# Kernel optimization log

Measured on AMD Instinct MI355X. Metric: run time of the kernel, lower is better.

## Reference

```python
import jax, jax.numpy as jnp
import numpy as np

N_HEAD = 12
N_EMBD = 768

def setup_inputs() -> dict:
    key = jax.random.key(0)
    ks = jax.random.split(key, 5)
    B, T, C = 4, 2048, N_EMBD
    x = jax.random.normal(ks[0], (B, T, C), dtype=jnp.float32)
    # PyTorch Linear default init ~ U(-1/sqrt(fan_in), 1/sqrt(fan_in)); use small normals for a clean baseline
    s = 1.0 / np.sqrt(C)
    W_attn = jax.random.uniform(ks[1], (C, 3 * C), minval=-s, maxval=s, dtype=jnp.float32)
    b_attn = jax.random.uniform(ks[2], (3 * C,), minval=-s, maxval=s, dtype=jnp.float32)
    W_o = jax.random.uniform(ks[3], (C, C), minval=-s, maxval=s, dtype=jnp.float32)
    b_o = jax.random.uniform(ks[4], (C,), minval=-s, maxval=s, dtype=jnp.float32)
    return {"x": x, "W_attn": W_attn, "b_attn": b_attn, "W_o": W_o, "b_o": b_o}

def reference(x, W_attn, b_attn, W_o, b_o):
    B, T, C = x.shape
    H = N_HEAD
    D = C // H  # head dim
    qkv = x @ W_attn + b_attn                      # [B,T,3C]
    q, k, v = jnp.split(qkv, 3, axis=-1)           # each [B,T,C]
    q = q.reshape(B, T, H, D).transpose(0, 2, 1, 3)  # [B,H,T,D]
    k = k.reshape(B, T, H, D).transpose(0, 2, 1, 3)
    v = v.reshape(B, T, H, D).transpose(0, 2, 1, 3)
    att = jnp.einsum('bhqd,bhkd->bhqk', q, k) / jnp.sqrt(jnp.asarray(D, x.dtype))
    causal = jnp.tril(jnp.ones((T, T), dtype=bool))
    att = jnp.where(causal, att, jnp.asarray(-jnp.inf, att.dtype))
    att = jax.nn.softmax(att, axis=-1)             # dropout=0.0 -> identity
    y = jnp.einsum('bhqk,bhkd->bhqd', att, v)      # [B,H,T,D]
    y = y.transpose(0, 2, 1, 3).reshape(B, T, C)   # [B,T,C]
    return y @ W_o + b_o
```

## Files before the change

kernel.cpp:

```cpp
#include <hip/hip_runtime.h>
#include <hip/hip_bf16.h>

#define NHEAD 12
#define TSEQ 2048
#define CEMB 768
#define DHEAD 64
#define NBATCH 4

typedef __attribute__((ext_vector_type(8))) short bf16x8;
typedef __attribute__((ext_vector_type(4))) float f32x4;

__device__ __forceinline__ ushort f2bf(float f) {
  union { float f; unsigned u; } v; v.f = f;
  unsigned u = v.u;
  u += 0x7FFFu + ((u >> 16) & 1u);
  return (ushort)(u >> 16);
}

__device__ __forceinline__ unsigned cvt_pk_bf16(float lo, float hi) {
  unsigned r;
  asm("v_cvt_pk_bf16_f32 %0, %1, %2" : "=v"(r) : "v"(lo), "v"(hi));
  return r;
}

__device__ __forceinline__ float exp2_raw(float x) {
  float r;
  asm("v_exp_f32 %0, %1" : "=v"(r) : "v"(x));
  return r;
}

__global__ __launch_bounds__(256)
void prep(const float* __restrict__ x, ushort* __restrict__ xb,
          const float* __restrict__ Wa, ushort* __restrict__ WaT,
          const float* __restrict__ Wo, ushort* __restrict__ WoT)
{
  __shared__ float tile[32][33];
  const int bid = blockIdx.x, t = threadIdx.x;
  if (bid < 3072) {
    int i = (bid * 256 + t) * 8;
    float4 v0 = *(const float4*)(x + i);
    float4 v1 = *(const float4*)(x + i + 4);
    bf16x8 wv;
    wv[0] = (short)f2bf(v0.x); wv[1] = (short)f2bf(v0.y);
    wv[2] = (short)f2bf(v0.z); wv[3] = (short)f2bf(v0.w);
    wv[4] = (short)f2bf(v1.x); wv[5] = (short)f2bf(v1.y);
    wv[6] = (short)f2bf(v1.z); wv[7] = (short)f2bf(v1.w);
    *(bf16x8*)(xb + i) = wv;
    return;
  }
  const int b2 = bid - 3072;
  const int bx = b2 % 96, by = b2 / 96;
  const int tx = t & 31, ty = t >> 5;
  const float* src; ushort* dst; int C, c0;
  if (bx < 72) { src = Wa; dst = WaT; C = 3 * CEMB; c0 = bx * 32; }
  else         { src = Wo; dst = WoT; C = CEMB;     c0 = (bx - 72) * 32; }
  const int r0 = by * 32;
#pragma unroll
  for (int j = 0; j < 4; ++j)
    tile[ty + j * 8][tx] = src[(size_t)(r0 + ty + j * 8) * C + c0 + tx];
  __syncthreads();
#pragma unroll
  for (int j = 0; j < 4; ++j)
    dst[(size_t)(c0 + ty + j * 8) * CEMB + r0 + tx] = f2bf(tile[tx][ty + j * 8]);
}

template<int EPI>
__global__ __launch_bounds__(256)
void gemm_bf16(const ushort* __restrict__ A, const ushort* __restrict__ BT,
               const float* __restrict__ bias, float* __restrict__ outF,
               ushort* __restrict__ qd, ushort* __restrict__ kd, ushort* __restrict__ vd,
               int M, int N, int K)
{
  __shared__ __align__(16) char smem[32768];
  const int t = threadIdx.x;
  const int lane = t & 63, wv = t >> 6;
  const int cc = lane & 15, gg = lane >> 4;
  const int m0 = blockIdx.y * 128, n0 = blockIdx.x * 128;
  const int wm = (wv >> 1) * 64, wn = (wv & 1) * 64;

  const int o0 = wv * 1024 + lane * 16;
  const int o1 = o0 + 4096;
  const int r0s = o0 >> 6, s0s = (o0 >> 4) & 3;
  const int r1s = o1 >> 6, s1s = (o1 >> 4) & 3;
  const size_t Kb = (size_t)K * 2;
  const char* a0p = (const char*)A  + (size_t)(m0 + r0s) * Kb + ((s0s ^ ((r0s >> 1) & 3)) << 4);
  const char* a1p = (const char*)A  + (size_t)(m0 + r1s) * Kb + ((s1s ^ ((r1s >> 1) & 3)) << 4);
  const char* b0p = (const char*)BT + (size_t)(n0 + r0s) * Kb + ((s0s ^ ((r0s >> 1) & 3)) << 4);
  const char* b1p = (const char*)BT + (size_t)(n0 + r1s) * Kb + ((s1s ^ ((r1s >> 1) & 3)) << 4);

  auto stage_g = [&](int p, int kb) {
    char* As = smem + p * 16384;
    char* Bs = As + 8192;
    __builtin_amdgcn_global_load_lds(
        (const __attribute__((address_space(1))) unsigned*)(a0p + kb),
        (__attribute__((address_space(3))) unsigned*)(As + wv * 1024), 16, 0, 0);
    __builtin_amdgcn_global_load_lds(
        (const __attribute__((address_space(1))) unsigned*)(a1p + kb),
        (__attribute__((address_space(3))) unsigned*)(As + wv * 1024 + 4096), 16, 0, 0);
    __builtin_amdgcn_global_load_lds(
        (const __attribute__((address_space(1))) unsigned*)(b0p + kb),
        (__attribute__((address_space(3))) unsigned*)(Bs + wv * 1024), 16, 0, 0);
    __builtin_amdgcn_global_load_lds(
        (const __attribute__((address_space(1))) unsigned*)(b1p + kb),
        (__attribute__((address_space(3))) unsigned*)(Bs + wv * 1024 + 4096), 16, 0, 0);
  };

  f32x4 acc[4][4];
#pragma unroll
  for (int i = 0; i < 4; ++i)
#pragma unroll
    for (int j = 0; j < 4; ++j) acc[i][j] = (f32x4){0.f, 0.f, 0.f, 0.f};

  const int KB = K * 2;
  stage_g(0, 0);
  asm volatile("s_waitcnt vmcnt(0)" ::: "memory");
  __syncthreads();
  int p = 0;
  for (int kb = 0; kb < KB; kb += 64) {
    if (kb + 64 < KB) stage_g(p ^ 1, kb + 64);
    const char* As = smem + p * 16384;
    const char* Bs = As + 8192;
    bf16x8 fa[4], fb[4];
#pragma unroll
    for (int i = 0; i < 4; ++i) {
      const int r = wm + i * 16 + cc;
      fa[i] = *(const bf16x8*)(As + r * 64 + ((gg ^ ((r >> 1) & 3)) << 4));
    }
#pragma unroll
    for (int j = 0; j < 4; ++j) {
      const int r = wn + j * 16 + cc;
      fb[j] = *(const bf16x8*)(Bs + r * 64 + ((gg ^ ((r >> 1) & 3)) << 4));
    }
    __builtin_amdgcn_s_setprio(1);
#pragma unroll
    for (int i = 0; i < 4; ++i)
#pragma unroll
      for (int j = 0; j < 4; ++j)
        acc[i][j] = __builtin_amdgcn_mfma_f32_16x16x32_bf16(fa[i], fb[j], acc[i][j], 0, 0, 0);
    __builtin_amdgcn_s_setprio(0);
    asm volatile("s_waitcnt vmcnt(0)" ::: "memory");
    __syncthreads();
    p ^= 1;
  }

#pragma unroll
  for (int i = 0; i < 4; ++i) {
#pragma unroll
    for (int j = 0; j < 4; ++j) {
      int gm0 = m0 + wm + i * 16 + gg * 4;
      int gn  = n0 + wn + j * 16 + cc;
      float bv = bias[gn];
      if (EPI == 0) {
#pragma unroll
        for (int e = 0; e < 4; ++e)
          outF[(size_t)(gm0 + e) * N + gn] = acc[i][j][e] + bv;
      } else {
        int which = gn / CEMB;
        int r = gn - which * CEMB;
        int hh = r >> 6, dd = r & 63;
        int tt0 = gm0 & (TSEQ - 1), bb = gm0 >> 11;
        if (which == 2) {
          ushort* dstv = vd + ((size_t)((bb * NHEAD + hh) * DHEAD + dd)) * TSEQ + tt0;
          uint2 pw;
          pw.x = cvt_pk_bf16(acc[i][j][0] + bv, acc[i][j][1] + bv);
          pw.y = cvt_pk_bf16(acc[i][j][2] + bv, acc[i][j][3] + bv);
          *(uint2*)dstv = pw;
        } else {
          ushort* dst = which == 0 ? qd : kd;
          float sc = (which == 0) ? 0.125f * 1.4426950408889634f : 1.0f;
#pragma unroll
          for (int e = 0; e < 4; ++e)
            dst[(size_t)((bb * NHEAD + hh) * TSEQ + tt0 + e) * DHEAD + dd] =
                f2bf((acc[i][j][e] + bv) * sc);
        }
      }
    }
  }
}

__global__ __launch_bounds__(256)
void attn_fwd(const ushort* __restrict__ qg, const ushort* __restrict__ kg,
              const ushort* __restrict__ vTg, ushort* __restrict__ ybb)
{
  __shared__ __align__(16) char smem[49152];
  const int t = threadIdx.x, lane = t & 63, w = t >> 6;
  const int cc = lane & 15, gg = lane >> 4;
  const int NT = TSEQ / 64;
  const int L = blockIdx.x;
  const int r9 = L >> 3;
  const int bx = r9 & 15;
  const int bh = (L & 7) + 8 * (r9 >> 4);
  const int b = bh / NHEAD, h = bh - b * NHEAD;

  const char* Kg = (const char*)(kg + (size_t)bh * TSEQ * DHEAD);
  const char* Vg = (const char*)(vTg + (size_t)bh * TSEQ * DHEAD);

  const int srow = lane >> 3;
  const int ssw  = ((lane & 7) * 16) ^ (srow << 4);

  ushort* Pw = (ushort*)(smem + 32768 + w * 4096);
  const int sw8 = (cc & 7) << 3;

  auto stageK = [&](int pb, int kt) {
#pragma unroll
    for (int i = 0; i < 2; ++i) {
      const int c = w * 2 + i;
      const char* gk = Kg + (size_t)(kt * 64 + c * 8 + srow) * 128 + ssw;
      __builtin_amdgcn_global_load_lds(
          (const __attribute__((address_space(1))) unsigned*)gk,
          (__attribute__((address_space(3))) unsigned*)(smem + pb * 8192 + c * 1024),
          16, 0, 0);
    }
  };
  auto stageV = [&](int pb, int kt) {
#pragma unroll
    for (int i = 0; i < 2; ++i) {
      const int c = w * 2 + i;
      const char* gv = Vg + (size_t)(c * 8 + srow) * (TSEQ * 2) + (size_t)kt * 128 + ssw;
      __builtin_amdgcn_global_load_lds(
          (const __attribute__((address_space(1))) unsigned*)gv,
          (__attribute__((address_space(3))) unsigned*)(smem + 16384 + pb * 8192 + c * 1024),
          16, 0, 0);
    }
  };

  int p = 0;
  for (int pass = 0; pass < 2; ++pass) {
    const int qt = pass ? (NT - 1 - bx) : bx;
    const int qrow0 = qt * 64 + w * 16;

    const ushort* Qp = qg + ((size_t)bh * TSEQ + qrow0) * DHEAD;
    bf16x8 fq0 = *(const bf16x8*)(Qp + cc * DHEAD + 8 * gg);
    bf16x8 fq1 = *(const bf16x8*)(Qp + cc * DHEAD + 32 + 8 * gg);

    f32x4 o[4];
#pragma unroll
    for (int i = 0; i < 4; ++i) o[i] = (f32x4){0.f, 0.f, 0.f, 0.f};
    float m = -1e30f, l = 0.f;

    stageK(p, 0);
    asm volatile("s_waitcnt vmcnt(0)" ::: "memory");
    __syncthreads();

    for (int kt = 0; kt <= qt; ++kt) {
      if (kt < qt) stageK(p ^ 1, kt + 1);
      stageV(p, kt);

      const char* Kl = smem + p * 8192;
      f32x4 st[4];
#pragma unroll
      for (int ct = 0; ct < 4; ++ct) st[ct] = (f32x4){0.f, 0.f, 0.f, 0.f};
      __builtin_amdgcn_s_setprio(1);
#pragma unroll
      for (int ct = 0; ct < 4; ++ct) {
        const int r = ct * 16 + cc;
        const char* kb = Kl + r * 128;
        bf16x8 fk0 = *(const bf16x8*)(kb + ((gg * 16) ^ ((r & 7) << 4)));
        bf16x8 fk1 = *(const bf16x8*)(kb + ((64 + gg * 16) ^ ((r & 7) << 4)));
        st[ct] = __builtin_amdgcn_mfma_f32_16x16x32_bf16(fk0, fq0, st[ct], 0, 0, 0);
        st[ct] = __builtin_amdgcn_mfma_f32_16x16x32_bf16(fk1, fq1, st[ct], 0, 0, 0);
      }

      if (kt > 0) {
        const char* Vprev = smem + 16384 + (p ^ 1) * 8192;
        const ushort* Pprev = Pw + (p ^ 1) * 1024;
#pragma unroll
        for (int kc = 0; kc < 2; ++kc) {
          bf16x8 pb = *(const bf16x8*)&Pprev[cc * 64 + ((kc * 32 + 8 * gg) ^ sw8)];
#pragma unroll
          for (int dt = 0; dt < 4; ++dt) {
            const int rd = dt * 16 + cc;
            bf16x8 fv = *(const bf16x8*)(Vprev + rd * 128 + ((kc * 64 + gg * 16) ^ ((rd & 7) << 4)));
            o[dt] = __builtin_amdgcn_mfma_f32_16x16x32_bf16(fv, pb, o[dt], 0, 0, 0);
          }
        }
      }
      __builtin_amdgcn_s_setprio(0);

      if (kt == qt) {
#pragma unroll
        for (int ct = 0; ct < 4; ++ct)
#pragma unroll
          for (int e = 0; e < 4; ++e)
            if (ct * 16 + gg * 4 + e > w * 16 + cc) st[ct][e] = -1e30f;
      }
      float ml = st[0][0];
#pragma unroll
      for (int ct = 0; ct < 4; ++ct)
#pragma unroll
        for (int e = 0; e < 4; ++e) ml = fmaxf(ml, st[ct][e]);
      ml = fmaxf(ml, __shfl_xor(ml, 16, 64));
      ml = fmaxf(ml, __shfl_xor(ml, 32, 64));
      float mn = m;
      if (!__all(ml - m <= 11.54f)) {
        mn = fmaxf(m, ml);
        float al = exp2_raw(m - mn);
#pragma unroll
        for (int dt = 0; dt < 4; ++dt)
#pragma unroll
          for (int e = 0; e < 4; ++e) o[dt][e] *= al;
        l *= al;
        m = mn;
      }
      float ps = 0.f;
#pragma unroll
      for (int ct = 0; ct < 4; ++ct)
#pragma unroll
        for (int e = 0; e < 4; ++e) { float pp = exp2_raw(st[ct][e] - mn); st[ct][e] = pp; ps += pp; }
#pragma unroll
      for (int ct = 0; ct < 4; ++ct) {
        uint2 pw;
        pw.x = cvt_pk_bf16(st[ct][0], st[ct][1]);
        pw.y = cvt_pk_bf16(st[ct][2], st[ct][3]);
        *(uint2*)&Pw[p * 1024 + cc * 64 + ((ct * 16 + gg * 4) ^ sw8)] = pw;
      }
      ps += __shfl_xor(ps, 16, 64);
      ps += __shfl_xor(ps, 32, 64);
      l += ps;

      asm volatile("s_waitcnt vmcnt(0)" ::: "memory");
      __syncthreads();
      p ^= 1;
    }

    {
      const char* Vlast = smem + 16384 + (p ^ 1) * 8192;
      const ushort* Plast = Pw + (p ^ 1) * 1024;
#pragma unroll
      for (int kc = 0; kc < 2; ++kc) {
        bf16x8 pb = *(const bf16x8*)&Plast[cc * 64 + ((kc * 32 + 8 * gg) ^ sw8)];
#pragma unroll
        for (int dt = 0; dt < 4; ++dt) {
          const int rd = dt * 16 + cc;
          bf16x8 fv = *(const bf16x8*)(Vlast + rd * 128 + ((kc * 64 + gg * 16) ^ ((rd & 7) << 4)));
          o[dt] = __builtin_amdgcn_mfma_f32_16x16x32_bf16(fv, pb, o[dt], 0, 0, 0);
        }
      }
    }

    float inv = 1.0f / l;
    ushort* yrow = ybb + (size_t)(b * TSEQ + qrow0 + cc) * CEMB + h * DHEAD;
#pragma unroll
    for (int dt = 0; dt < 4; ++dt) {
      uint2 pw;
      pw.x = cvt_pk_bf16(o[dt][0] * inv, o[dt][1] * inv);
      pw.y = cvt_pk_bf16(o[dt][2] * inv, o[dt][3] * inv);
      *(uint2*)(yrow + dt * 16 + gg * 4) = pw;
    }
  }
}

extern "C" void kernel_launch(void* const* d_in, const int* in_sizes, int n_in,
                              void* d_out, int out_size, void* d_ws, size_t ws_size,
                              hipStream_t stream)
{
  (void)in_sizes; (void)n_in; (void)out_size; (void)ws_size;
  const float* x  = (const float*)d_in[0];
  const float* Wa = (const float*)d_in[1];
  const float* ba = (const float*)d_in[2];
  const float* Wo = (const float*)d_in[3];
  const float* bo = (const float*)d_in[4];
  float* out = (float*)d_out;

  char* p = (char*)d_ws;
  ushort* WaT  = (ushort*)p; p += (size_t)3 * CEMB * CEMB * 2;
  ushort* WoT  = (ushort*)p; p += (size_t)CEMB * CEMB * 2;
  ushort* xb   = (ushort*)p; p += (size_t)NBATCH * TSEQ * CEMB * 2;
  ushort* qb   = (ushort*)p; p += (size_t)NBATCH * NHEAD * TSEQ * DHEAD * 2;
  ushort* kb   = (ushort*)p; p += (size_t)NBATCH * NHEAD * TSEQ * DHEAD * 2;
  ushort* vT   = (ushort*)p; p += (size_t)NBATCH * NHEAD * TSEQ * DHEAD * 2;
  ushort* yb   = (ushort*)p; p += (size_t)NBATCH * TSEQ * CEMB * 2;

  prep<<<3072 + 96 * 24, 256, 0, stream>>>(x, xb, Wa, WaT, Wo, WoT);
  gemm_bf16<1><<<dim3(3 * CEMB / 128, NBATCH * TSEQ / 128), 256, 0, stream>>>(
      xb, WaT, ba, nullptr, qb, kb, vT, NBATCH * TSEQ, 3 * CEMB, CEMB);
  attn_fwd<<<dim3(TSEQ / 128 * NBATCH * NHEAD), 256, 0, stream>>>(qb, kb, vT, yb);
  gemm_bf16<0><<<dim3(CEMB / 128, NBATCH * TSEQ / 128), 256, 0, stream>>>(
      yb, WoT, bo, out, nullptr, nullptr, nullptr, NBATCH * TSEQ, CEMB, CEMB);
}
```

Baseline: 132.7 us.

## Compute softmax row sums with MFMA and exponentiate before max reduction

The softmax denominator is now accumulated by an extra MFMA that multiplies a ones vector by the bf16 probability tile, replacing the per-lane sum and its two cross-lane shuffles. Exponentials are computed against the previous running max and written to LDS before the new max is reduced, with a rescale-and-rewrite path only when the max grows past the threshold. This shortens the dependency chain between the QK^T result and the P store. The trade is two extra MFMAs per tile, a redundant P write on rescale, and a row sum taken from bf16-rounded P, which also makes the running max start at 0 instead of a large negative value.

Measured after the change: 132.4 us. Within noise of the previous version (-0.2%).

```diff
diff --git a/kernel.cpp b/kernel.cpp
--- a/kernel.cpp
+++ b/kernel.cpp
@@ -201,6 +201,10 @@
   ushort* Pw = (ushort*)(smem + 32768 + w * 4096);
   const int sw8 = (cc & 7) << 3;
 
+  bf16x8 ones;
+#pragma unroll
+  for (int i = 0; i < 8; ++i) ones[i] = (short)0x3F80;
+
   auto stageK = [&](int pb, int kt) {
 #pragma unroll
     for (int i = 0; i < 2; ++i) {
@@ -234,9 +238,10 @@
     bf16x8 fq1 = *(const bf16x8*)(Qp + cc * DHEAD + 32 + 8 * gg);
 
     f32x4 o[4];
+    f32x4 l4 = (f32x4){0.f, 0.f, 0.f, 0.f};
 #pragma unroll
     for (int i = 0; i < 4; ++i) o[i] = (f32x4){0.f, 0.f, 0.f, 0.f};
-    float m = -1e30f, l = 0.f;
+    float m = 0.f;
 
     stageK(p, 0);
     asm volatile("s_waitcnt vmcnt(0)" ::: "memory");
@@ -267,6 +272,7 @@
 #pragma unroll
         for (int kc = 0; kc < 2; ++kc) {
           bf16x8 pb = *(const bf16x8*)&Pprev[cc * 64 + ((kc * 32 + 8 * gg) ^ sw8)];
+          l4 = __builtin_amdgcn_mfma_f32_16x16x32_bf16(ones, pb, l4, 0, 0, 0);
 #pragma unroll
           for (int dt = 0; dt < 4; ++dt) {
             const int rd = dt * 16 + cc;
@@ -284,39 +290,46 @@
           for (int e = 0; e < 4; ++e)
             if (ct * 16 + gg * 4 + e > w * 16 + cc) st[ct][e] = -1e30f;
       }
-      float ml = st[0][0];
+      f32x4 pe[4];
 #pragma unroll
       for (int ct = 0; ct < 4; ++ct)
 #pragma unroll
-        for (int e = 0; e < 4; ++e) ml = fmaxf(ml, st[ct][e]);
+        for (int e = 0; e < 4; ++e) pe[ct][e] = exp2_raw(st[ct][e] - m);
+#pragma unroll
+      for (int ct = 0; ct < 4; ++ct) {
+        uint2 pw;
+        pw.x = cvt_pk_bf16(pe[ct][0], pe[ct][1]);
+        pw.y = cvt_pk_bf16(pe[ct][2], pe[ct][3]);
+        *(uint2*)&Pw[p * 1024 + cc * 64 + ((ct * 16 + gg * 4) ^ sw8)] = pw;
+      }
+      float ml = fmaxf(fmaxf(st[0][0], st[0][1]), st[0][2]);
+      ml = fmaxf(fmaxf(ml, st[0][3]), fmaxf(st[1][0], st[1][1]));
+      ml = fmaxf(fmaxf(ml, st[1][2]), fmaxf(st[1][3], st[2][0]));
+      ml = fmaxf(fmaxf(ml, st[2][1]), fmaxf(st[2][2], st[2][3]));
+      ml = fmaxf(fmaxf(ml, st[3][0]), fmaxf(st[3][1], st[3][2]));
+      ml = fmaxf(ml, st[3][3]);
       ml = fmaxf(ml, __shfl_xor(ml, 16, 64));
       ml = fmaxf(ml, __shfl_xor(ml, 32, 64));
-      float mn = m;
       if (!__all(ml - m <= 11.54f)) {
-        mn = fmaxf(m, ml);
+        float mn = fmaxf(m, ml);
         float al = exp2_raw(m - mn);
 #pragma unroll
         for (int dt = 0; dt < 4; ++dt)
 #pragma unroll
           for (int e = 0; e < 4; ++e) o[dt][e] *= al;
-        l *= al;
+#pragma unroll
+        for (int e = 0; e < 4; ++e) l4[e] *= al;
+#pragma unroll
+        for (int ct = 0; ct < 4; ++ct) {
+#pragma unroll
+          for (int e = 0; e < 4; ++e) pe[ct][e] *= al;
+          uint2 pw;
+          pw.x = cvt_pk_bf16(pe[ct][0], pe[ct][1]);
+          pw.y = cvt_pk_bf16(pe[ct][2], pe[ct][3]);
+          *(uint2*)&Pw[p * 1024 + cc * 64 + ((ct * 16 + gg * 4) ^ sw8)] = pw;
+        }
         m = mn;
       }
-      float ps = 0.f;
-#pragma unroll
-      for (int ct = 0; ct < 4; ++ct)
-#pragma unroll
-        for (int e = 0; e < 4; ++e) { float pp = exp2_raw(st[ct][e] - mn); st[ct][e] = pp; ps += pp; }
-#pragma unroll
-      for (int ct = 0; ct < 4; ++ct) {
-        uint2 pw;
-        pw.x = cvt_pk_bf16(st[ct][0], st[ct][1]);
-        pw.y = cvt_pk_bf16(st[ct][2], st[ct][3]);
-        *(uint2*)&Pw[p * 1024 + cc * 64 + ((ct * 16 + gg * 4) ^ sw8)] = pw;
-      }
-      ps += __shfl_xor(ps, 16, 64);
-      ps += __shfl_xor(ps, 32, 64);
-      l += ps;
 
       asm volatile("s_waitcnt vmcnt(0)" ::: "memory");
       __syncthreads();
@@ -329,6 +342,7 @@
 #pragma unroll
       for (int kc = 0; kc < 2; ++kc) {
         bf16x8 pb = *(const bf16x8*)&Plast[cc * 64 + ((kc * 32 + 8 * gg) ^ sw8)];
+        l4 = __builtin_amdgcn_mfma_f32_16x16x32_bf16(ones, pb, l4, 0, 0, 0);
 #pragma unroll
         for (int dt = 0; dt < 4; ++dt) {
           const int rd = dt * 16 + cc;
@@ -338,7 +352,7 @@
       }
     }
 
-    float inv = 1.0f / l;
+    float inv = 1.0f / l4[0];
     ushort* yrow = ybb + (size_t)(b * TSEQ + qrow0 + cc) * CEMB + h * DHEAD;
 #pragma unroll
     for (int dt = 0; dt < 4; ++dt) {
```
